# Performance work log

Hardware: AMD Instinct MI355X
Metric: run time of the kernel (lower is better)

## Reference

```python
import jax, jax.numpy as jnp
import numpy as np
from jax import lax

B = 64            # batch size
IMG = 128         # image H=W
C_IN = 3          # channels (also conv kernel size in original code)
Q_DIM = 11
A_DIM = 10
CONV = [24, 24, 24, 24]
KS = 3
EPS = 1e-5
G_IN = (CONV[-1] + 2) * 2 + Q_DIM  # 63


def _lin_init(key, fin, fout):
    kw, kb = jax.random.split(key)
    w = jax.random.normal(kw, (fin, fout), jnp.float32) / np.sqrt(fin).astype(np.float32)
    b = jax.random.normal(kb, (fout,), jnp.float32) * 0.01
    return w, b


def _conv_init(key, cin, cout):
    kw, kb = jax.random.split(key)
    w = jax.random.normal(kw, (cout, cin, KS, KS), jnp.float32) / np.sqrt(cin * KS * KS).astype(np.float32)
    b = jax.random.normal(kb, (cout,), jnp.float32) * 0.01
    return w, b


def setup_inputs() -> dict:
    key = jax.random.key(0)
    ks = jax.random.split(key, 16)
    inp = {
        'img': jax.random.normal(ks[0], (B, C_IN, IMG, IMG), jnp.float32),
        'q': jax.random.normal(ks[1], (B, Q_DIM), jnp.float32),
    }
    cins = [C_IN] + CONV[:-1]
    for li in range(4):
        w, b = _conv_init(ks[2 + li], cins[li], CONV[li])
        inp[f'cw{li+1}'], inp[f'cb{li+1}'] = w, b
        inp[f'bg{li+1}'] = jnp.ones((CONV[li],), jnp.float32)
        inp[f'bb{li+1}'] = jnp.zeros((CONV[li],), jnp.float32)
    gins = [G_IN, 256, 256, 256]
    for li in range(4):
        w, b = _lin_init(ks[6 + li], gins[li], 256)
        inp[f'gw{li+1}'], inp[f'gb{li+1}'] = w, b
    fins, fouts = [256, 256, 256], [256, 256, A_DIM]
    for li in range(3):
        w, b = _lin_init(ks[10 + li], fins[li], fouts[li])
        inp[f'fw{li+1}'], inp[f'fb{li+1}'] = w, b
    return inp


def _conv_block(x, w, b, g, bb):
    # conv(stride=2, pad=1) -> relu -> batchnorm (train-mode batch stats)
    x = lax.conv_general_dilated(x, w, (2, 2), [(1, 1), (1, 1)],
                                 dimension_numbers=('NCHW', 'OIHW', 'NCHW'))
    x = jax.nn.relu(x + b[None, :, None, None])
    m = jnp.mean(x, axis=(0, 2, 3), keepdims=True)
    v = jnp.var(x, axis=(0, 2, 3), keepdims=True)
    return g[None, :, None, None] * (x - m) * jax.lax.rsqrt(v + EPS) + bb[None, :, None, None]


def _forward(img, q,
             cw1, cb1, bg1, bb1, cw2, cb2, bg2, bb2,
             cw3, cb3, bg3, bb3, cw4, cb4, bg4, bb4,
             gw1, gb1, gw2, gb2, gw3, gb3, gw4, gb4,
             fw1, fb1, fw2, fb2, fw3, fb3):
    x = _conv_block(img, cw1, cb1, bg1, bb1)
    x = _conv_block(x, cw2, cb2, bg2, bb2)
    x = _conv_block(x, cw3, cb3, bg3, bb3)
    x = _conv_block(x, cw4, cb4, bg4, bb4)        # [B, K, d, d]
    d = x.shape[2]
    N = d * d
    Kc = x.shape[1]
    # objects: o at flat index i corresponds to pixel (i//d, i%d) -> row-major reshape
    objs = x.reshape(B, Kc, N).transpose(0, 2, 1)           # [B, N, K]
    idx = jnp.arange(N)
    coords = jnp.stack([(idx // d).astype(jnp.float32) / d,
                        (idx % d).astype(jnp.float32) / d], axis=1)  # [N, 2]
    o = jnp.concatenate([objs, jnp.broadcast_to(coords[None], (B, N, 2))], axis=-1)  # [B, N, K+2]
    F = Kc + 2
    oi = jnp.broadcast_to(o[:, :, None, :], (B, N, N, F))
    oj = jnp.broadcast_to(o[:, None, :, :], (B, N, N, F))
    qb = jnp.broadcast_to(q[:, None, None, :], (B, N, N, Q_DIM))
    pair = jnp.concatenate([oi, oj, qb], axis=-1)           # [B, N, N, 2F+Q]
    h = jax.nn.relu(jnp.einsum('bijf,fh->bijh', pair, gw1) + gb1)
    h = jax.nn.relu(h @ gw2 + gb2)
    h = jax.nn.relu(h @ gw3 + gb3)
    h = jax.nn.relu(h @ gw4 + gb4)
    g = jnp.mean(h, axis=(1, 2))                            # mean over all N*N pairs -> [B, 256]
    # f_phi (dropout as identity / eval mode)
    g = jax.nn.relu(g @ fw1 + fb1)
    g = jax.nn.relu(g @ fw2 + fb2)
    logits = g @ fw3 + fb3
    return logits


def reference(img, q,
              cw1, cb1, bg1, bb1, cw2, cb2, bg2, bb2,
              cw3, cb3, bg3, bb3, cw4, cb4, bg4, bb4,
              gw1, gb1, gw2, gb2, gw3, gb3, gw4, gb4,
              fw1, fb1, fw2, fb2, fw3, fb3):
    return _forward(img, q,
                    cw1, cb1, bg1, bb1, cw2, cb2, bg2, bb2,
                    cw3, cb3, bg3, bb3, cw4, cb4, bg4, bb4,
                    gw1, gb1, gw2, gb2, gw3, gb3, gw4, gb4,
                    fw1, fb1, fw2, fb2, fw3, fb3)
```

## Files before the change

### kernel.cpp

```cpp
#include <hip/hip_runtime.h>
#include <hip/hip_bf16.h>

#define EPS_BN 1e-5f

typedef __bf16 bf16_t;
typedef __bf16 bf16x8 __attribute__((ext_vector_type(8)));
typedef float floatx16 __attribute__((ext_vector_type(16)));

__global__ __launch_bounds__(256) void prep_kernel(
    const float* __restrict__ q, const float* __restrict__ gw1,
    const float* __restrict__ gb1, const float* __restrict__ g2,
    const float* __restrict__ g3, const float* __restrict__ g4,
    float* __restrict__ wq, bf16_t* __restrict__ wpack)
{
    int blk = blockIdx.x, t = threadIdx.x;
    {
        float acc = gb1[t];
        #pragma unroll
        for (int d = 0; d < 11; d++)
            acc = fmaf(q[blk * 11 + d], gw1[(52 + d) * 256 + t], acc);
        wq[blk * 256 + t] = acc;
    }
    for (int idx = blk * 3072 + t; idx < blk * 3072 + 3072; idx += 256) {
        int layer = idx >> 16;
        int rem = idx & 65535;
        int col = rem & 255;
        int k = rem >> 8;
        const float* gw = (layer == 0) ? g2 : ((layer == 1) ? g3 : g4);
        float v = gw[k * 256 + col];
        int cg = col >> 5, l31 = col & 31;
        int kt = k >> 4, l2 = (k >> 3) & 1, e = k & 7;
        int lane = l2 * 32 + l31;
        wpack[(((layer * 8 + cg) * 16 + kt) * 64 + lane) * 8 + e] = (bf16_t)v;
    }
}

__global__ __launch_bounds__(256) void fin_kernel(
    const float* __restrict__ part, int P, float inv_n,
    const float* __restrict__ gamma, const float* __restrict__ beta,
    float* __restrict__ scsh)
{
    int c = blockIdx.x;
    int t = threadIdx.x;
    float s1 = 0.f, s2 = 0.f;
    for (int p = t; p < P; p += 256) {
        s1 += part[p * 48 + 2 * c];
        s2 += part[p * 48 + 2 * c + 1];
    }
    #pragma unroll
    for (int off = 32; off > 0; off >>= 1) {
        s1 += __shfl_xor(s1, off);
        s2 += __shfl_xor(s2, off);
    }
    __shared__ float r1[4], r2[4];
    int lane = t & 63, w = t >> 6;
    if (lane == 0) { r1[w] = s1; r2[w] = s2; }
    __syncthreads();
    if (t == 0) {
        float a1 = r1[0] + r1[1] + r1[2] + r1[3];
        float a2 = r2[0] + r2[1] + r2[2] + r2[3];
        float m = a1 * inv_n;
        float var = a2 * inv_n - m * m;
        float sc = gamma[c] * rsqrtf(var + EPS_BN);
        scsh[c] = sc;
        scsh[24 + c] = fmaf(-m, sc, beta[c]);
    }
}

template<int CIN, int HOUT, int OY_PER, int CO_PER, bool FOLD>
__global__ __launch_bounds__(256) void conv_kernel(
    const float* __restrict__ in, const float* __restrict__ scsh_in,
    const float* __restrict__ w, const float* __restrict__ bias,
    float* __restrict__ out, float* __restrict__ part_out)
{
    const int HIN = 2 * HOUT, ROWS = 2 * OY_PER + 3, RW = 2 * HOUT + 2;
    const int TILES = HOUT / OY_PER;
    const int WPC = (HOUT * OY_PER) / 64;
    int b = blockIdx.x / TILES, tile = blockIdx.x % TILES;
    int oy0 = tile * OY_PER;
    __shared__ float tin[CIN][ROWS][RW];
    __shared__ float scf[24], shf[24];
    __shared__ float red[4][CO_PER * 2];
    int t = threadIdx.x;
    if (FOLD) {
        if (t < 24) { scf[t] = scsh_in[t]; shf[t] = scsh_in[24 + t]; }
        __syncthreads();
    }
    const int total = CIN * ROWS * RW;
    int iyb = 2 * oy0 - 1;
    #pragma unroll 2
    for (int idx = t; idx < total; idx += 256) {
        int rx = idx % RW;
        int rem = idx / RW;
        int ry = rem % ROWS;
        int ci = rem / ROWS;
        int iy = iyb + ry, ix = rx - 1;
        float v = 0.f;
        if ((unsigned)iy < (unsigned)HIN && (unsigned)ix < (unsigned)HIN) {
            float raw = in[(b * CIN + ci) * HIN * HIN + iy * HIN + ix];
            v = FOLD ? fmaf(raw, scf[ci], shf[ci]) : raw;
        }
        tin[ci][ry][rx] = v;
    }
    __syncthreads();
    int ox = t % HOUT;
    int oyl = (t / HOUT) % OY_PER;
    int cog = t / (HOUT * OY_PER);
    const float* wp = w + cog * CO_PER * CIN * 9;
    float acc[CO_PER];
    #pragma unroll
    for (int r = 0; r < CO_PER; r++) acc[r] = bias[cog * CO_PER + r];
    for (int ci = 0; ci < CIN; ci++)
        #pragma unroll
        for (int ky = 0; ky < 3; ky++)
            #pragma unroll
            for (int kx = 0; kx < 3; kx++) {
                float v = tin[ci][2 * oyl + ky][2 * ox + kx];
                #pragma unroll
                for (int r = 0; r < CO_PER; r++)
                    acc[r] = fmaf(v, wp[(r * CIN + ci) * 9 + ky * 3 + kx], acc[r]);
            }
    int oy = oy0 + oyl;
    float s1[CO_PER], s2[CO_PER];
    #pragma unroll
    for (int r = 0; r < CO_PER; r++) {
        float v = fmaxf(acc[r], 0.f);
        out[((b * 24 + cog * CO_PER + r) * HOUT + oy) * HOUT + ox] = v;
        s1[r] = v;
        s2[r] = v * v;
    }
    int lane = t & 63, w_id = t >> 6;
    #pragma unroll
    for (int r = 0; r < CO_PER; r++) {
        float a = s1[r], c2 = s2[r];
        #pragma unroll
        for (int off = 32; off > 0; off >>= 1) {
            a += __shfl_xor(a, off);
            c2 += __shfl_xor(c2, off);
        }
        if (lane == 0) { red[w_id][r * 2] = a; red[w_id][r * 2 + 1] = c2; }
    }
    __syncthreads();
    if (t < 48) {
        int ch = t >> 1, st = t & 1;
        int cg = ch / CO_PER, r = ch % CO_PER;
        float v = 0.f;
        #pragma unroll
        for (int k = 0; k < WPC; k++) v += red[cg * WPC + k][r * 2 + st];
        part_out[blockIdx.x * 48 + t] = v;
    }
}

__global__ __launch_bounds__(256) void uv_kernel(
    const float* __restrict__ x4, const float* __restrict__ scsh4,
    const float* __restrict__ gw1, float* __restrict__ U, float* __restrict__ V)
{
    int b = blockIdx.x >> 2, n0 = (blockIdx.x & 3) * 16;
    __shared__ float o[16][26];
    int t = threadIdx.x;
    for (int idx = t; idx < 16 * 26; idx += 256) {
        int n = idx / 26, f = idx % 26;
        int ng = n0 + n;
        float val;
        if (f < 24)
            val = fmaf(x4[(b * 24 + f) * 64 + ng], scsh4[f], scsh4[24 + f]);
        else if (f == 24) val = (float)(ng >> 3) * 0.125f;
        else              val = (float)(ng & 7) * 0.125f;
        o[n][f] = val;
    }
    __syncthreads();
    float g1u[26], g1v[26];
    #pragma unroll
    for (int f = 0; f < 26; f++) {
        g1u[f] = gw1[f * 256 + t];
        g1v[f] = gw1[(26 + f) * 256 + t];
    }
    for (int n = 0; n < 16; n++) {
        float u = 0.f, v = 0.f;
        #pragma unroll
        for (int f = 0; f < 26; f++) {
            float of = o[n][f];
            u = fmaf(of, g1u[f], u);
            v = fmaf(of, g1v[f], v);
        }
        int ng = n0 + n;
        U[(b * 64 + ng) * 256 + t] = u;
        V[(b * 64 + ng) * 256 + t] = v;
    }
}

__global__ __launch_bounds__(512, 4) void pair_kernel(
    const float* __restrict__ U, const float* __restrict__ V,
    const float* __restrict__ wq, const bf16_t* __restrict__ wpack,
    const float* __restrict__ gb2, const float* __restrict__ gb3,
    const float* __restrict__ gb4, float* __restrict__ partial)
{
    __shared__ __align__(16) bf16_t hA[128][264];
    __shared__ float csum[2][256];
    int blk = blockIdx.x;
    int b = blk >> 5;
    int i0 = (blk & 31) * 2;
    int t = threadIdx.x;

    {
        int c = t & 255, jh = t >> 8;
        float wqc = wq[b * 256 + c];
        float uw0 = U[(b * 64 + i0) * 256 + c] + wqc;
        float uw1 = U[(b * 64 + i0 + 1) * 256 + c] + wqc;
        const float* Vb = V + (b * 64) * 256;
        for (int j = jh * 32; j < jh * 32 + 32; j++) {
            float v = Vb[j * 256 + c];
            hA[j][c]      = (bf16_t)fmaxf(uw0 + v, 0.0f);
            hA[64 + j][c] = (bf16_t)fmaxf(uw1 + v, 0.0f);
        }
    }
    __syncthreads();

    int lane = t & 63, wave = t >> 6;
    int wm = wave >> 2, wn = wave & 3;
    int l31 = lane & 31, l2 = lane >> 5;
    int r0 = wm * 64 + l31;
    const floatx16 zero16 = {0.f, 0.f, 0.f, 0.f, 0.f, 0.f, 0.f, 0.f,
                             0.f, 0.f, 0.f, 0.f, 0.f, 0.f, 0.f, 0.f};
    float colsum[2] = {0.f, 0.f};

    #pragma unroll 1
    for (int layer = 0; layer < 3; layer++) {
        const float* bias = (layer == 0) ? gb2 : ((layer == 1) ? gb3 : gb4);
        float bcol[2];
        #pragma unroll
        for (int nt = 0; nt < 2; nt++)
            bcol[nt] = bias[wn * 64 + nt * 32 + l31];

        floatx16 acc[2][2];
        #pragma unroll
        for (int mt = 0; mt < 2; mt++)
            #pragma unroll
            for (int nt = 0; nt < 2; nt++) acc[mt][nt] = zero16;

        const bf16_t* W0 = wpack + ((size_t)(layer * 8 + wn * 2) * 16 * 64 + lane) * 8;
        const bf16_t* W1 = W0 + (size_t)16 * 64 * 8;
        bf16x8 Bc[2];
        Bc[0] = *(const bf16x8*)W0;
        Bc[1] = *(const bf16x8*)W1;

        #pragma unroll
        for (int ks = 0; ks < 16; ks++) {
            bf16x8 Bn[2];
            if (ks < 15) {
                Bn[0] = *(const bf16x8*)(W0 + (ks + 1) * 64 * 8);
                Bn[1] = *(const bf16x8*)(W1 + (ks + 1) * 64 * 8);
            }
            bf16x8 a0 = *(const bf16x8*)&hA[r0][ks * 16 + l2 * 8];
            bf16x8 a1 = *(const bf16x8*)&hA[r0 + 32][ks * 16 + l2 * 8];
            #pragma unroll
            for (int nt = 0; nt < 2; nt++) {
                acc[0][nt] = __builtin_amdgcn_mfma_f32_32x32x16_bf16(a0, Bc[nt], acc[0][nt], 0, 0, 0);
                acc[1][nt] = __builtin_amdgcn_mfma_f32_32x32x16_bf16(a1, Bc[nt], acc[1][nt], 0, 0, 0);
            }
            if (ks < 15) { Bc[0] = Bn[0]; Bc[1] = Bn[1]; }
        }

        if (layer < 2) {
            __syncthreads();
            #pragma unroll
            for (int mt = 0; mt < 2; mt++)
                #pragma unroll
                for (int nt = 0; nt < 2; nt++) {
                    int col = wn * 64 + nt * 32 + l31;
                    #pragma unroll
                    for (int reg = 0; reg < 16; reg++) {
                        int row = wm * 64 + mt * 32 + (reg & 3) + 8 * (reg >> 2) + 4 * l2;
                        hA[row][col] = (bf16_t)fmaxf(acc[mt][nt][reg] + bcol[nt], 0.0f);
                    }
                }
            __syncthreads();
        } else {
            #pragma unroll
            for (int nt = 0; nt < 2; nt++) {
                float s = 0.f;
                #pragma unroll
                for (int mt = 0; mt < 2; mt++)
                    #pragma unroll
                    for (int reg = 0; reg < 16; reg++)
                        s += fmaxf(acc[mt][nt][reg] + bcol[nt], 0.0f);
                colsum[nt] += s;
            }
        }
    }

    #pragma unroll
    for (int nt = 0; nt < 2; nt++)
        colsum[nt] += __shfl_xor(colsum[nt], 32);
    if (l2 == 0) {
        #pragma unroll
        for (int nt = 0; nt < 2; nt++)
            csum[wm][wn * 64 + nt * 32 + l31] = colsum[nt];
    }
    __syncthreads();
    if (t < 256)
        partial[blk * 256 + t] = csum[0][t] + csum[1][t];
}

__global__ __launch_bounds__(256) void fphi_kernel(
    const float* __restrict__ partial,
    const float* __restrict__ fw1, const float* __restrict__ fb1,
    const float* __restrict__ fw2, const float* __restrict__ fb2,
    const float* __restrict__ fw3, const float* __restrict__ fb3,
    float* __restrict__ out)
{
    int b = blockIdx.x, t = threadIdx.x;
    __shared__ float g[256], h1[256], h2[256];
    float s = 0.f;
    for (int k = 0; k < 32; k++) s += partial[(b * 32 + k) * 256 + t];
    g[t] = s * (1.0f / 4096.0f);
    __syncthreads();
    float a1 = fb1[t];
    for (int k = 0; k < 256; k++) a1 = fmaf(g[k], fw1[k * 256 + t], a1);
    h1[t] = fmaxf(a1, 0.0f);
    __syncthreads();
    float a2 = fb2[t];
    for (int k = 0; k < 256; k++) a2 = fmaf(h1[k], fw2[k * 256 + t], a2);
    h2[t] = fmaxf(a2, 0.0f);
    __syncthreads();
    if (t < 10) {
        float a3 = fb3[t];
        for (int k = 0; k < 256; k++) a3 = fmaf(h2[k], fw3[k * 10 + t], a3);
        out[b * 10 + t] = a3;
    }
}

extern "C" void kernel_launch(void* const* d_in, const int* in_sizes, int n_in,
                              void* d_out, int out_size, void* d_ws, size_t ws_size,
                              hipStream_t stream)
{
    (void)in_sizes; (void)n_in; (void)out_size; (void)ws_size;
    const float* img = (const float*)d_in[0];
    const float* q   = (const float*)d_in[1];
    const float* cw[4] = {(const float*)d_in[2],  (const float*)d_in[6],
                          (const float*)d_in[10], (const float*)d_in[14]};
    const float* cb[4] = {(const float*)d_in[3],  (const float*)d_in[7],
                          (const float*)d_in[11], (const float*)d_in[15]};
    const float* bg[4] = {(const float*)d_in[4],  (const float*)d_in[8],
                          (const float*)d_in[12], (const float*)d_in[16]};
    const float* bbv[4] = {(const float*)d_in[5],  (const float*)d_in[9],
                           (const float*)d_in[13], (const float*)d_in[17]};
    const float* gw1 = (const float*)d_in[18]; const float* gb1 = (const float*)d_in[19];
    const float* gw2 = (const float*)d_in[20]; const float* gb2 = (const float*)d_in[21];
    const float* gw3 = (const float*)d_in[22]; const float* gb3 = (const float*)d_in[23];
    const float* gw4 = (const float*)d_in[24]; const float* gb4 = (const float*)d_in[25];
    const float* fw1 = (const float*)d_in[26]; const float* fb1 = (const float*)d_in[27];
    const float* fw2 = (const float*)d_in[28]; const float* fb2 = (const float*)d_in[29];
    const float* fw3 = (const float*)d_in[30]; const float* fb3 = (const float*)d_in[31];

    float* ws  = (float*)d_ws;
    float* x1  = ws;
    float* x2  = x1 + 6291456;
    float* x3  = x2 + 1572864;
    float* x4  = x3 + 393216;
    float* U   = x4 + 98304;
    float* V   = U + 1048576;
    float* wqv = V + 1048576;
    float* part = wqv + 16384;
    float* p1  = part + 524288;
    float* p2  = p1 + 98304;
    float* p3  = p2 + 49152;
    float* p4  = p3 + 12288;
    float* scsh1 = p4 + 3072;
    float* scsh2 = scsh1 + 48;
    float* scsh3 = scsh2 + 48;
    float* scsh4 = scsh3 + 48;
    bf16_t* wpack = (bf16_t*)(scsh4 + 48);

    prep_kernel<<<64, 256, 0, stream>>>(q, gw1, gb1, gw2, gw3, gw4, wqv, wpack);
    conv_kernel<3, 64, 2, 12, false><<<2048, 256, 0, stream>>>(
        img, nullptr, cw[0], cb[0], x1, p1);
    fin_kernel<<<24, 256, 0, stream>>>(p1, 2048, 1.f / 262144.f, bg[0], bbv[0], scsh1);
    conv_kernel<24, 32, 2, 6, true><<<1024, 256, 0, stream>>>(
        x1, scsh1, cw[1], cb[1], x2, p2);
    fin_kernel<<<24, 256, 0, stream>>>(p2, 1024, 1.f / 65536.f, bg[1], bbv[1], scsh2);
    conv_kernel<24, 16, 4, 6, true><<<256, 256, 0, stream>>>(
        x2, scsh2, cw[2], cb[2], x3, p3);
    fin_kernel<<<24, 256, 0, stream>>>(p3, 256, 1.f / 16384.f, bg[2], bbv[2], scsh3);
    conv_kernel<24, 8, 8, 6, true><<<64, 256, 0, stream>>>(
        x3, scsh3, cw[3], cb[3], x4, p4);
    fin_kernel<<<24, 256, 0, stream>>>(p4, 64, 1.f / 4096.f, bg[3], bbv[3], scsh4);
    uv_kernel<<<256, 256, 0, stream>>>(x4, scsh4, gw1, U, V);
    pair_kernel<<<2048, 512, 0, stream>>>(U, V, wqv, wpack, gb2, gb3, gb4, part);
    fphi_kernel<<<64, 256, 0, stream>>>(part, fw1, fb1, fw2, fb2, fw3, fb3,
                                        (float*)d_out);
}
```

Before: 441.6 us.

## Transpose MFMA operands for hidden layers to write activations as vector stores

For the first two g_theta hidden layers, the MFMA operands are swapped so weights act as A and activations as B. Each wave then owns one 32-row tile across 128 features. The output lands with features contiguous per lane, so the bias+ReLU writeback to shared memory becomes 4-wide bf16 stores instead of scattered scalar stores. The initial pair-activation fill also moves to float4 loads and bf16x4 stores. This trades more register pressure (four accumulators and four prefetched weight fragments) for fewer LDS store instructions and possibly fewer bank conflicts.

New measurement: 440.8 us. No clear change (-0.2%).

```diff
diff --git a/kernel.cpp b/kernel.cpp
--- a/kernel.cpp
+++ b/kernel.cpp
@@ -4,6 +4,7 @@
 #define EPS_BN 1e-5f
 
 typedef __bf16 bf16_t;
+typedef __bf16 bf16x4 __attribute__((ext_vector_type(4)));
 typedef __bf16 bf16x8 __attribute__((ext_vector_type(8)));
 typedef float floatx16 __attribute__((ext_vector_type(16)));
 
@@ -203,34 +204,94 @@
     int t = threadIdx.x;
 
     {
-        int c = t & 255, jh = t >> 8;
-        float wqc = wq[b * 256 + c];
-        float uw0 = U[(b * 64 + i0) * 256 + c] + wqc;
-        float uw1 = U[(b * 64 + i0 + 1) * 256 + c] + wqc;
-        const float* Vb = V + (b * 64) * 256;
-        for (int j = jh * 32; j < jh * 32 + 32; j++) {
-            float v = Vb[j * 256 + c];
-            hA[j][c]      = (bf16_t)fmaxf(uw0 + v, 0.0f);
-            hA[64 + j][c] = (bf16_t)fmaxf(uw1 + v, 0.0f);
+        int c4 = (t & 63) * 4;
+        int jh = t >> 6;
+        float4 wq4 = *(const float4*)(wq + b * 256 + c4);
+        float4 u0 = *(const float4*)(U + (b * 64 + i0) * 256 + c4);
+        float4 u1 = *(const float4*)(U + (b * 64 + i0 + 1) * 256 + c4);
+        u0.x += wq4.x; u0.y += wq4.y; u0.z += wq4.z; u0.w += wq4.w;
+        u1.x += wq4.x; u1.y += wq4.y; u1.z += wq4.z; u1.w += wq4.w;
+        const float* Vb = V + (b * 64) * 256 + c4;
+        for (int j = jh * 8; j < jh * 8 + 8; j++) {
+            float4 v = *(const float4*)(Vb + j * 256);
+            bf16x4 h0, h1;
+            h0[0] = (bf16_t)fmaxf(u0.x + v.x, 0.f);
+            h0[1] = (bf16_t)fmaxf(u0.y + v.y, 0.f);
+            h0[2] = (bf16_t)fmaxf(u0.z + v.z, 0.f);
+            h0[3] = (bf16_t)fmaxf(u0.w + v.w, 0.f);
+            h1[0] = (bf16_t)fmaxf(u1.x + v.x, 0.f);
+            h1[1] = (bf16_t)fmaxf(u1.y + v.y, 0.f);
+            h1[2] = (bf16_t)fmaxf(u1.z + v.z, 0.f);
+            h1[3] = (bf16_t)fmaxf(u1.w + v.w, 0.f);
+            *(bf16x4*)&hA[j][c4] = h0;
+            *(bf16x4*)&hA[64 + j][c4] = h1;
         }
     }
     __syncthreads();
 
     int lane = t & 63, wave = t >> 6;
-    int wm = wave >> 2, wn = wave & 3;
     int l31 = lane & 31, l2 = lane >> 5;
-    int r0 = wm * 64 + l31;
     const floatx16 zero16 = {0.f, 0.f, 0.f, 0.f, 0.f, 0.f, 0.f, 0.f,
                              0.f, 0.f, 0.f, 0.f, 0.f, 0.f, 0.f, 0.f};
+
+    int fg = wave >> 2;
+    int rt = wave & 3;
+    int row = rt * 32 + l31;
+    #pragma unroll 1
+    for (int layer = 0; layer < 2; layer++) {
+        const float* bias = (layer == 0) ? gb2 : gb3;
+        const bf16_t* Wb = wpack + ((size_t)((layer * 8 + fg * 4) * 1024) + lane) * 8;
+        bf16x8 Bc[4], Bn[4];
+        #pragma unroll
+        for (int nt = 0; nt < 4; nt++)
+            Bc[nt] = *(const bf16x8*)(Wb + nt * 8192);
+        floatx16 acc[4];
+        #pragma unroll
+        for (int nt = 0; nt < 4; nt++) acc[nt] = zero16;
+
+        #pragma unroll
+        for (int ks = 0; ks < 16; ks++) {
+            if (ks < 15) {
+                #pragma unroll
+                for (int nt = 0; nt < 4; nt++)
+                    Bn[nt] = *(const bf16x8*)(Wb + nt * 8192 + (ks + 1) * 512);
+            }
+            bf16x8 hb = *(const bf16x8*)&hA[row][ks * 16 + l2 * 8];
+            #pragma unroll
+            for (int nt = 0; nt < 4; nt++)
+                acc[nt] = __builtin_amdgcn_mfma_f32_32x32x16_bf16(Bc[nt], hb, acc[nt], 0, 0, 0);
+            if (ks < 15) {
+                #pragma unroll
+                for (int nt = 0; nt < 4; nt++) Bc[nt] = Bn[nt];
+            }
+        }
+
+        __syncthreads();
+        #pragma unroll
+        for (int nt = 0; nt < 4; nt++) {
+            int fb = fg * 128 + nt * 32 + 4 * l2;
+            #pragma unroll
+            for (int g = 0; g < 4; g++) {
+                float4 bv = *(const float4*)(bias + fb + 8 * g);
+                bf16x4 w4;
+                w4[0] = (bf16_t)fmaxf(acc[nt][4 * g + 0] + bv.x, 0.f);
+                w4[1] = (bf16_t)fmaxf(acc[nt][4 * g + 1] + bv.y, 0.f);
+                w4[2] = (bf16_t)fmaxf(acc[nt][4 * g + 2] + bv.z, 0.f);
+                w4[3] = (bf16_t)fmaxf(acc[nt][4 * g + 3] + bv.w, 0.f);
+                *(bf16x4*)&hA[row][fb + 8 * g] = w4;
+            }
+        }
+        __syncthreads();
+    }
+
+    int wm = wave >> 2, wn = wave & 3;
+    int r0 = wm * 64 + l31;
     float colsum[2] = {0.f, 0.f};
-
-    #pragma unroll 1
-    for (int layer = 0; layer < 3; layer++) {
-        const float* bias = (layer == 0) ? gb2 : ((layer == 1) ? gb3 : gb4);
+    {
         float bcol[2];
         #pragma unroll
         for (int nt = 0; nt < 2; nt++)
-            bcol[nt] = bias[wn * 64 + nt * 32 + l31];
+            bcol[nt] = gb4[wn * 64 + nt * 32 + l31];
 
         floatx16 acc[2][2];
         #pragma unroll
@@ -238,54 +299,37 @@
             #pragma unroll
             for (int nt = 0; nt < 2; nt++) acc[mt][nt] = zero16;
 
-        const bf16_t* W0 = wpack + ((size_t)(layer * 8 + wn * 2) * 16 * 64 + lane) * 8;
-        const bf16_t* W1 = W0 + (size_t)16 * 64 * 8;
-        bf16x8 Bc[2];
-        Bc[0] = *(const bf16x8*)W0;
-        Bc[1] = *(const bf16x8*)W1;
+        const bf16_t* W0 = wpack + ((size_t)((16 + wn * 2) * 1024) + lane) * 8;
+        const bf16_t* W1 = W0 + 8192;
+        bf16x8 Bc2[2], Bn2[2];
+        Bc2[0] = *(const bf16x8*)W0;
+        Bc2[1] = *(const bf16x8*)W1;
 
         #pragma unroll
         for (int ks = 0; ks < 16; ks++) {
-            bf16x8 Bn[2];
             if (ks < 15) {
-                Bn[0] = *(const bf16x8*)(W0 + (ks + 1) * 64 * 8);
-                Bn[1] = *(const bf16x8*)(W1 + (ks + 1) * 64 * 8);
+                Bn2[0] = *(const bf16x8*)(W0 + (ks + 1) * 512);
+                Bn2[1] = *(const bf16x8*)(W1 + (ks + 1) * 512);
             }
             bf16x8 a0 = *(const bf16x8*)&hA[r0][ks * 16 + l2 * 8];
             bf16x8 a1 = *(const bf16x8*)&hA[r0 + 32][ks * 16 + l2 * 8];
             #pragma unroll
             for (int nt = 0; nt < 2; nt++) {
-                acc[0][nt] = __builtin_amdgcn_mfma_f32_32x32x16_bf16(a0, Bc[nt], acc[0][nt], 0, 0, 0);
-                acc[1][nt] = __builtin_amdgcn_mfma_f32_32x32x16_bf16(a1, Bc[nt], acc[1][nt], 0, 0, 0);
-            }
-            if (ks < 15) { Bc[0] = Bn[0]; Bc[1] = Bn[1]; }
-        }
-
-        if (layer < 2) {
-            __syncthreads();
+                acc[0][nt] = __builtin_amdgcn_mfma_f32_32x32x16_bf16(a0, Bc2[nt], acc[0][nt], 0, 0, 0);
+                acc[1][nt] = __builtin_amdgcn_mfma_f32_32x32x16_bf16(a1, Bc2[nt], acc[1][nt], 0, 0, 0);
+            }
+            if (ks < 15) { Bc2[0] = Bn2[0]; Bc2[1] = Bn2[1]; }
+        }
+
+        #pragma unroll
+        for (int nt = 0; nt < 2; nt++) {
+            float s = 0.f;
             #pragma unroll
             for (int mt = 0; mt < 2; mt++)
                 #pragma unroll
-                for (int nt = 0; nt < 2; nt++) {
-                    int col = wn * 64 + nt * 32 + l31;
-                    #pragma unroll
-                    for (int reg = 0; reg < 16; reg++) {
-                        int row = wm * 64 + mt * 32 + (reg & 3) + 8 * (reg >> 2) + 4 * l2;
-                        hA[row][col] = (bf16_t)fmaxf(acc[mt][nt][reg] + bcol[nt], 0.0f);
-                    }
-                }
-            __syncthreads();
-        } else {
-            #pragma unroll
-            for (int nt = 0; nt < 2; nt++) {
-                float s = 0.f;
-                #pragma unroll
-                for (int mt = 0; mt < 2; mt++)
-                    #pragma unroll
-                    for (int reg = 0; reg < 16; reg++)
-                        s += fmaxf(acc[mt][nt][reg] + bcol[nt], 0.0f);
-                colsum[nt] += s;
-            }
+                for (int reg = 0; reg < 16; reg++)
+                    s += fmaxf(acc[mt][nt][reg] + bcol[nt], 0.0f);
+            colsum[nt] += s;
         }
     }
 
```
